# Kernel optimization log

Hardware: AMD Instinct MI355X
Metric: run time of the kernel (lower is better)

The kernel has to match this reference:

```python
import jax, jax.numpy as jnp
import numpy as np

H = 4   # num_attention_heads
C = 32  # attention_head_size
LN_EPS = 1e-5

def setup_inputs() -> dict:
    key = jax.random.key(0)
    ks = jax.random.split(key, 8)
    E = 128  # embedding_channels; all_head_size = H*C = 128
    B, I, J = 1, 256, 256
    s = 1.0 / np.sqrt(E)
    return {
        "z": jax.random.normal(ks[0], (B, I, J, E), dtype=jnp.float32),
        "ln_scale": jnp.ones((E,), jnp.float32),
        "ln_bias": jnp.zeros((E,), jnp.float32),
        # weights stored as [in, out] (torch Linear applies x @ W.T; here y = x @ W)
        "Wq": jax.random.normal(ks[1], (E, H * C), jnp.float32) * s,
        "Wk": jax.random.normal(ks[2], (E, H * C), jnp.float32) * s,
        "Wv": jax.random.normal(ks[3], (E, H * C), jnp.float32) * s,
        "Wg": jax.random.normal(ks[4], (E, H * C), jnp.float32) * s,
        "bg": jnp.zeros((H * C,), jnp.float32),
        "Wo": jax.random.normal(ks[5], (H * C, E), jnp.float32) * s,
        "bo": jnp.zeros((E,), jnp.float32),
    }

def reference(z, ln_scale, ln_bias, Wq, Wk, Wv, Wg, bg, Wo, bo):
    B, I, J, E = z.shape
    # LayerNorm over last dim
    mu = jnp.mean(z, axis=-1, keepdims=True)
    var = jnp.mean(jnp.square(z - mu), axis=-1, keepdims=True)
    zn = (z - mu) * jax.lax.rsqrt(var + LN_EPS) * ln_scale + ln_bias
    # QKV projections, reshaped to heads: [B, I, J, H, C]
    q = (zn @ Wq).reshape(B, I, J, H, C)
    k = (zn @ Wk).reshape(B, I, J, H, C)
    v = (zn @ Wv).reshape(B, I, J, H, C)
    # Row-wise attention (NOTE: original has no 1/sqrt(c) scaling)
    logits = jnp.einsum('biqhc,bikhc->bihqk', q, k)  # [B, I, H, J, J]
    weights = jax.nn.softmax(logits, axis=-1)
    wavg = jnp.einsum('bihqk,bikhc->biqhc', weights, v)  # [B, I, J, H, C]
    # Sigmoid gate
    g = jax.nn.sigmoid((zn @ Wg + bg).reshape(B, I, J, H, C))
    out = (g * wavg).reshape(B, I, J, H * C)
    return out @ Wo + bo
```

## Files before the change

kernel.cpp:

```cpp
#include <hip/hip_runtime.h>

typedef unsigned short u16;
typedef unsigned int   u32;
using bf16x8 = __attribute__((ext_vector_type(8))) __bf16;
using f32x4  = __attribute__((ext_vector_type(4))) float;

#define MFMA16(a,b,c) __builtin_amdgcn_mfma_f32_16x16x32_bf16(a,b,c,0,0,0)

__device__ __forceinline__ float b2f(u16 u){ u32 x = ((u32)u) << 16; return __builtin_bit_cast(float, x); }
__device__ __forceinline__ u16 f2b(float f){
    u32 x = __builtin_bit_cast(u32, f);
    return (u16)((x + 0x7fffu + ((x >> 16) & 1u)) >> 16);
}
__device__ __forceinline__ u32 pk2(float a, float b){ return (u32)f2b(a) | ((u32)f2b(b) << 16); }

constexpr int LDB = 136;
constexpr int LDK = 40;
constexpr int LDV = 264;
constexpr int LDQ = 40;
constexpr int LDZ = 136;
constexpr int LDT = 20;

__global__ __launch_bounds__(256) void kw_prep(
    const float* __restrict__ Wq, const float* __restrict__ Wk,
    const float* __restrict__ Wv, const float* __restrict__ Wg,
    const float* __restrict__ Wo, u16* __restrict__ Wt)
{
    const int m = blockIdx.x >> 4;
    const int r = ((blockIdx.x & 15) << 8) | threadIdx.x;
    const int o  = r >> 5;
    const int e4 = (r & 31) << 2;
    const float* __restrict__ src;
    bool lo = false;
    switch (m) {
        case 0: src = Wq; break;
        case 1: src = Wk; break;
        case 2: src = Wv; break;
        case 3: src = Wg; break;
        case 4: src = Wq; lo = true; break;
        case 5: src = Wk; lo = true; break;
        default: src = Wo; break;
    }
    float w[4];
    #pragma unroll
    for (int i = 0; i < 4; ++i) w[i] = src[(e4 + i) * 128 + o];
    if (lo) {
        #pragma unroll
        for (int i = 0; i < 4; ++i) w[i] -= b2f(f2b(w[i]));
    }
    uint2 outv;
    outv.x = pk2(w[0], w[1]);
    outv.y = pk2(w[2], w[3]);
    *(uint2*)(Wt + m * 16384 + o * 128 + e4) = outv;
}

__global__ __launch_bounds__(512, 2) void k1_proj(
    const float* __restrict__ z, const float* __restrict__ lns, const float* __restrict__ lnb,
    const u16* __restrict__ Wt, const float* __restrict__ bg,
    u16* __restrict__ Qo, u16* __restrict__ Ko, u16* __restrict__ Vo, u16* __restrict__ Go)
{
    __shared__ __attribute__((aligned(16))) u16 bufA[128 * LDB];
    __shared__ __attribute__((aligned(16))) u16 bufB[128 * LDB];
    __shared__ __attribute__((aligned(16))) u16 ett[8 * 16 * LDT];

    const int t = threadIdx.x;
    const int lane = t & 63;
    const int l15  = lane & 15;
    const int quad = lane >> 4;
    const int wave = t >> 6;
    const int rowbase = blockIdx.x * 128 + wave * 16;
    u16* __restrict__ lntile = bufA + wave * 16 * LDZ;
    u16* __restrict__ myE = ett + wave * 16 * LDT;

    bf16x8 zfh[4], zfl[4];
    {
        float sc[32], bi[32];
        #pragma unroll
        for (int u = 0; u < 8; ++u) {
            float4 s4 = *(const float4*)(lns + quad * 32 + u * 4);
            float4 b4 = *(const float4*)(lnb + quad * 32 + u * 4);
            sc[u*4+0]=s4.x; sc[u*4+1]=s4.y; sc[u*4+2]=s4.z; sc[u*4+3]=s4.w;
            bi[u*4+0]=b4.x; bi[u*4+1]=b4.y; bi[u*4+2]=b4.z; bi[u*4+3]=b4.w;
        }
        const size_t tok = (size_t)(rowbase + l15);
        float x[32];
        #pragma unroll
        for (int u = 0; u < 8; ++u) {
            float4 v4 = *(const float4*)(z + (tok << 7) + quad * 32 + u * 4);
            x[u*4+0]=v4.x; x[u*4+1]=v4.y; x[u*4+2]=v4.z; x[u*4+3]=v4.w;
        }
        float s = 0.f;
        #pragma unroll
        for (int k = 0; k < 32; ++k) s += x[k];
        s += __shfl_xor(s, 16, 64); s += __shfl_xor(s, 32, 64);
        const float mu = s * 0.0078125f;
        float vs = 0.f;
        #pragma unroll
        for (int k = 0; k < 32; ++k) { float d = x[k] - mu; vs += d * d; }
        vs += __shfl_xor(vs, 16, 64); vs += __shfl_xor(vs, 32, 64);
        const float rs = rsqrtf(vs * 0.0078125f + 1e-5f);
        float y[32];
        #pragma unroll
        for (int k = 0; k < 32; ++k) y[k] = (x[k] - mu) * rs * sc[k] + bi[k];
        #pragma unroll
        for (int u = 0; u < 4; ++u) {
            uint4 o;
            o.x = pk2(y[u*8+0], y[u*8+1]); o.y = pk2(y[u*8+2], y[u*8+3]);
            o.z = pk2(y[u*8+4], y[u*8+5]); o.w = pk2(y[u*8+6], y[u*8+7]);
            *(uint4*)(lntile + l15 * LDZ + quad * 32 + u * 8) = o;
        }
        #pragma unroll
        for (int ks = 0; ks < 4; ++ks)
            zfh[ks] = *(const bf16x8*)(lntile + l15 * LDZ + ks * 32 + quad * 8);
        #pragma unroll
        for (int k = 0; k < 32; ++k) y[k] -= b2f(f2b(y[k]));
        #pragma unroll
        for (int u = 0; u < 4; ++u) {
            uint4 o;
            o.x = pk2(y[u*8+0], y[u*8+1]); o.y = pk2(y[u*8+2], y[u*8+3]);
            o.z = pk2(y[u*8+4], y[u*8+5]); o.w = pk2(y[u*8+6], y[u*8+7]);
            *(uint4*)(lntile + l15 * LDZ + quad * 32 + u * 8) = o;
        }
        #pragma unroll
        for (int ks = 0; ks < 4; ++ks)
            zfl[ks] = *(const bf16x8*)(lntile + l15 * LDZ + ks * 32 + quad * 8);
    }

    auto stage = [&](u16* __restrict__ buf, const u16* __restrict__ src) {
        #pragma unroll
        for (int u = 0; u < 4; ++u) {
            const int c = (t + u * 512) * 8;
            *(uint4*)(buf + (c >> 7) * LDB + (c & 127)) = *(const uint4*)(src + c);
        }
    };

    u16* Os[4] = {Qo, Ko, Vo, Go};

    #pragma unroll 1
    for (int g = 0; g < 4; ++g) {
        __syncthreads();
        stage(bufA, Wt + g * 16384);
        const bool three = (g < 2);
        if (three) stage(bufB, Wt + (4 + g) * 16384);
        __syncthreads();
        u16* __restrict__ O = Os[g];
        #pragma unroll
        for (int nt = 0; nt < 8; ++nt) {
            f32x4 ac = {0.f, 0.f, 0.f, 0.f};
            const int bbase = (nt * 16 + l15) * LDB + quad * 8;
            #pragma unroll
            for (int ks = 0; ks < 4; ++ks) {
                bf16x8 bh = *(const bf16x8*)(bufA + bbase + ks * 32);
                ac = MFMA16(zfh[ks], bh, ac);
                if (three) {
                    bf16x8 bl = *(const bf16x8*)(bufB + bbase + ks * 32);
                    ac = MFMA16(zfl[ks], bh, ac);
                    ac = MFMA16(zfh[ks], bl, ac);
                }
            }
            const int col = nt * 16 + l15;
            #pragma unroll
            for (int r = 0; r < 4; ++r) {
                float v = ac[r];
                if (g == 3) v = 1.f / (1.f + __expf(-(v + bg[col])));
                myE[(quad * 4 + r) * LDT + l15] = f2b(v);
            }
            uint2 w = *(const uint2*)(myE + l15 * LDT + quad * 4);
            *(uint2*)(O + ((size_t)(rowbase + l15) << 7) + nt * 16 + quad * 4) = w;
        }
    }
}

__global__ __launch_bounds__(512, 4) void k2_attn(
    u16* QG, const u16* __restrict__ K, const u16* __restrict__ V)
{
    __shared__ __attribute__((aligned(16))) u16 kh[256 * 64];
    __shared__ __attribute__((aligned(16))) u16 vt[64 * LDV];
    __shared__ __attribute__((aligned(16))) u16 ptt[8 * 16 * LDQ];

    const int bid = blockIdx.x;
    const int i = bid >> 1, hp = bid & 1;
    const int t = threadIdx.x;
    const int lane = t & 63;
    const int l15  = lane & 15;
    const int quad = lane >> 4;
    const int wave = t >> 6;
    u16* __restrict__ myT = ptt + wave * 16 * LDQ;
    const size_t rb = ((size_t)i) << 8;
    const int cb = hp * 64;

    {
        const int tok = t >> 1, half = t & 1;
        const int swz = (tok & 7) << 3;
        const u16* ksrc = K + ((rb + tok) << 7) + cb + half * 32;
        #pragma unroll
        for (int u = 0; u < 4; ++u)
            *(uint4*)(kh + tok * 64 + ((half * 32 + u * 8) ^ swz)) = *(const uint4*)(ksrc + u * 8);
        const u16* vsrc = V + ((rb + tok) << 7) + cb + half * 32;
        #pragma unroll
        for (int u = 0; u < 4; ++u) {
            uint4 q = *(const uint4*)(vsrc + u * 8);
            u32 w4[4] = {q.x, q.y, q.z, q.w};
            #pragma unroll
            for (int k2 = 0; k2 < 4; ++k2) {
                vt[(half * 32 + u * 8 + k2 * 2    ) * LDV + tok] = (u16)(w4[k2] & 0xffffu);
                vt[(half * 32 + u * 8 + k2 * 2 + 1) * LDV + tok] = (u16)(w4[k2] >> 16);
            }
        }
    }
    __syncthreads();

    #pragma unroll 1
    for (int it = 0; it < 2; ++it) {
        u32 gwlo[2][4], gwhi[2][4];
        #pragma unroll
        for (int hh = 0; hh < 2; ++hh) {
            const int hc = cb + hh * 32;
            bf16x8 aq = *(const bf16x8*)(QG + ((rb + wave * 32 + it * 16 + l15) << 7) + hc + quad * 8);

            f32x4 s[16];
            #pragma unroll
            for (int nt = 0; nt < 16; ++nt) {
                const int key = nt * 16 + l15;
                bf16x8 b = *(const bf16x8*)(kh + key * 64 + ((hh * 32 + quad * 8) ^ ((key & 7) << 3)));
                f32x4 zacc = {0.f, 0.f, 0.f, 0.f};
                s[nt] = MFMA16(aq, b, zacc);
            }
            float inv[4];
            #pragma unroll
            for (int r = 0; r < 4; ++r) {
                float mx = s[0][r];
                #pragma unroll
                for (int nt = 1; nt < 16; ++nt) mx = fmaxf(mx, s[nt][r]);
                #pragma unroll
                for (int m = 1; m < 16; m <<= 1) mx = fmaxf(mx, __shfl_xor(mx, m, 64));
                float sm = 0.f;
                #pragma unroll
                for (int nt = 0; nt < 16; ++nt) {
                    float e = __expf(s[nt][r] - mx);
                    s[nt][r] = e; sm += e;
                }
                #pragma unroll
                for (int m = 1; m < 16; m <<= 1) sm += __shfl_xor(sm, m, 64);
                inv[r] = 1.f / sm;
            }
            f32x4 o0 = {0.f,0.f,0.f,0.f}, o1 = {0.f,0.f,0.f,0.f};
            #pragma unroll
            for (int c8 = 0; c8 < 8; ++c8) {
                #pragma unroll
                for (int n2 = 0; n2 < 2; ++n2)
                    #pragma unroll
                    for (int r = 0; r < 4; ++r)
                        myT[(quad * 4 + r) * LDQ + n2 * 16 + l15] = f2b(s[c8 * 2 + n2][r]);
                bf16x8 a  = *(const bf16x8*)(myT + l15 * LDQ + quad * 8);
                bf16x8 b0 = *(const bf16x8*)(vt + (hh * 32 +      l15) * LDV + c8 * 32 + quad * 8);
                bf16x8 b1 = *(const bf16x8*)(vt + (hh * 32 + 16 + l15) * LDV + c8 * 32 + quad * 8);
                o0 = MFMA16(a, b0, o0);
                o1 = MFMA16(a, b1, o1);
            }
            #pragma unroll
            for (int r = 0; r < 4; ++r) {
                gwlo[hh][r] = f2b(o0[r] * inv[r]);
                gwhi[hh][r] = f2b(o1[r] * inv[r]);
            }
        }
        #pragma unroll
        for (int r = 0; r < 4; ++r) {
            u16* dst = QG + ((rb + wave * 32 + it * 16 + quad * 4 + r) << 7) + cb;
            dst[     l15] = (u16)gwlo[0][r];
            dst[16 + l15] = (u16)gwhi[0][r];
            dst[32 + l15] = (u16)gwlo[1][r];
            dst[48 + l15] = (u16)gwhi[1][r];
        }
    }
}

__global__ __launch_bounds__(256, 4) void k3_out(
    const u16* __restrict__ GW, const u16* __restrict__ Gb,
    const u16* __restrict__ WoT, const float* __restrict__ bo,
    float* __restrict__ out)
{
    __shared__ __attribute__((aligned(16))) u16 wt[128 * LDB];
    __shared__ __attribute__((aligned(16))) float ftt[4 * 16 * LDT];
    const int t = threadIdx.x;
    const int lane = t & 63;
    const int l15  = lane & 15;
    const int quad = lane >> 4;
    const int wave = t >> 6;
    const int rowbase = blockIdx.x * 64 + wave * 16;
    float* __restrict__ myF = ftt + wave * 16 * LDT;

    #pragma unroll
    for (int u = 0; u < 8; ++u) {
        const int c = (t + u * 256) * 8;
        *(uint4*)(wt + (c >> 7) * LDB + (c & 127)) = *(const uint4*)(WoT + c);
    }
    bf16x8 af[4];
    {
        const size_t rowoff = (size_t)(rowbase + l15) << 7;
        #pragma unroll
        for (int ks = 0; ks < 4; ++ks) {
            bf16x8 a = *(const bf16x8*)(GW + rowoff + ks * 32 + quad * 8);
            bf16x8 g = *(const bf16x8*)(Gb + rowoff + ks * 32 + quad * 8);
            const u32* au = (const u32*)&a;
            const u32* gu = (const u32*)&g;
            u32 w[4];
            #pragma unroll
            for (int j = 0; j < 4; ++j) {
                float lo = b2f((u16)(au[j] & 0xffffu)) * b2f((u16)(gu[j] & 0xffffu));
                float hi = b2f((u16)(au[j] >> 16))     * b2f((u16)(gu[j] >> 16));
                w[j] = pk2(lo, hi);
            }
            af[ks] = *(const bf16x8*)w;
        }
    }
    __syncthreads();

    #pragma unroll
    for (int nt = 0; nt < 8; ++nt) {
        f32x4 ac = {0.f, 0.f, 0.f, 0.f};
        const int bbase = (nt * 16 + l15) * LDB + quad * 8;
        #pragma unroll
        for (int ks = 0; ks < 4; ++ks) {
            bf16x8 b = *(const bf16x8*)(wt + bbase + ks * 32);
            ac = MFMA16(af[ks], b, ac);
        }
        const float bb = bo[nt * 16 + l15];
        #pragma unroll
        for (int r = 0; r < 4; ++r)
            myF[(quad * 4 + r) * LDT + l15] = ac[r] + bb;
        float4 w = *(const float4*)(myF + l15 * LDT + quad * 4);
        *(float4*)(out + ((size_t)(rowbase + l15) << 7) + nt * 16 + quad * 4) = w;
    }
}

constexpr int FLDZ = 136;
constexpr int FLDW = 136;
constexpr int FLDO = 40;

__global__ __launch_bounds__(512, 2) void k_fused(
    const float* __restrict__ z, const float* __restrict__ lns, const float* __restrict__ lnb,
    const float* __restrict__ Wq, const float* __restrict__ Wk, const float* __restrict__ Wv,
    const float* __restrict__ Wg, const float* __restrict__ bg,
    const float* __restrict__ Wo, const float* __restrict__ bo,
    float* __restrict__ out)
{
    __shared__ __attribute__((aligned(16))) u16 smem[33280];
    const int i = blockIdx.x;
    const int t = threadIdx.x;
    const int lane = t & 63;
    const int l15  = lane & 15;
    const int quad = lane >> 4;
    const int wave = t >> 6;
    u16* __restrict__ kh   = smem;
    u16* __restrict__ vt   = smem + 10240;
    u16* __restrict__ bufA = smem + 18688;
    u16* __restrict__ myT  = smem + 23808 + wave * 16 * LDQ;
    u16* __restrict__ bufB = smem + 28928;
    u16* __restrict__ lntile = smem + wave * 16 * FLDZ;

    float4 wregA[2], wregB[2];
    auto prefW = [&](const float* __restrict__ W, int h, float4 (&r)[2]) {
        #pragma unroll
        for (int k2 = 0; k2 < 2; ++k2) {
            const int c = t * 4 + k2 * 2048;
            r[k2] = *(const float4*)(W + (c >> 5) * 128 + h * 32 + (c & 31));
        }
    };
    auto prefWoF = [&](int h, float4 (&r)[2]) {
        #pragma unroll
        for (int k2 = 0; k2 < 2; ++k2)
            r[k2] = *(const float4*)(Wo + h * 4096 + t * 4 + k2 * 2048);
    };
    auto stageHi = [&](u16* __restrict__ buf, const float4 (&r)[2]) {
        #pragma unroll
        for (int k2 = 0; k2 < 2; ++k2) {
            const int c = t * 4 + k2 * 2048;
            const int e = c >> 5, o = c & 31;
            buf[(o    ) * FLDW + e] = f2b(r[k2].x);
            buf[(o + 1) * FLDW + e] = f2b(r[k2].y);
            buf[(o + 2) * FLDW + e] = f2b(r[k2].z);
            buf[(o + 3) * FLDW + e] = f2b(r[k2].w);
        }
    };
    auto stageLo = [&](u16* __restrict__ buf, const float4 (&r)[2]) {
        #pragma unroll
        for (int k2 = 0; k2 < 2; ++k2) {
            const int c = t * 4 + k2 * 2048;
            const int e = c >> 5, o = c & 31;
            const float v0 = r[k2].x, v1 = r[k2].y, v2 = r[k2].z, v3 = r[k2].w;
            buf[(o    ) * FLDW + e] = f2b(v0 - b2f(f2b(v0)));
            buf[(o + 1) * FLDW + e] = f2b(v1 - b2f(f2b(v1)));
            buf[(o + 2) * FLDW + e] = f2b(v2 - b2f(f2b(v2)));
            buf[(o + 3) * FLDW + e] = f2b(v3 - b2f(f2b(v3)));
        }
    };
    auto stageWoL = [&](const float4 (&r)[2]) {
        #pragma unroll
        for (int k2 = 0; k2 < 2; ++k2) {
            const int c = t * 4 + k2 * 2048;
            const int kk = c >> 7, n = c & 127;
            bufA[(n    ) * FLDO + kk] = f2b(r[k2].x);
            bufA[(n + 1) * FLDO + kk] = f2b(r[k2].y);
            bufA[(n + 2) * FLDO + kk] = f2b(r[k2].z);
            bufA[(n + 3) * FLDO + kk] = f2b(r[k2].w);
        }
    };
    prefW(Wq, 0, wregA);
    bf16x8 zfh[2][4], zfl[2][4];
    {
        float sc[32], bi[32];
        #pragma unroll
        for (int u = 0; u < 8; ++u) {
            float4 s4 = *(const float4*)(lns + quad * 32 + u * 4);
            float4 b4 = *(const float4*)(lnb + quad * 32 + u * 4);
            sc[u*4+0]=s4.x; sc[u*4+1]=s4.y; sc[u*4+2]=s4.z; sc[u*4+3]=s4.w;
            bi[u*4+0]=b4.x; bi[u*4+1]=b4.y; bi[u*4+2]=b4.z; bi[u*4+3]=b4.w;
        }
        #pragma unroll 1
        for (int ms = 0; ms < 2; ++ms) {
            const size_t tok = (size_t)(i * 256 + wave * 32 + ms * 16 + l15);
            float x[32];
            #pragma unroll
            for (int u = 0; u < 8; ++u) {
                float4 v4 = *(const float4*)(z + (tok << 7) + quad * 32 + u * 4);
                x[u*4+0]=v4.x; x[u*4+1]=v4.y; x[u*4+2]=v4.z; x[u*4+3]=v4.w;
            }
            float s = 0.f;
            #pragma unroll
            for (int k = 0; k < 32; ++k) s += x[k];
            s += __shfl_xor(s, 16, 64); s += __shfl_xor(s, 32, 64);
            const float mu = s * 0.0078125f;
            float vs = 0.f;
            #pragma unroll
            for (int k = 0; k < 32; ++k) { float d = x[k] - mu; vs += d * d; }
            vs += __shfl_xor(vs, 16, 64); vs += __shfl_xor(vs, 32, 64);
            const float rs = rsqrtf(vs * 0.0078125f + 1e-5f);
            float y[32];
            #pragma unroll
            for (int k = 0; k < 32; ++k) y[k] = (x[k] - mu) * rs * sc[k] + bi[k];
            #pragma unroll
            for (int u = 0; u < 4; ++u) {
                uint4 o;
                o.x = pk2(y[u*8+0], y[u*8+1]); o.y = pk2(y[u*8+2], y[u*8+3]);
                o.z = pk2(y[u*8+4], y[u*8+5]); o.w = pk2(y[u*8+6], y[u*8+7]);
                *(uint4*)(lntile + l15 * FLDZ + quad * 32 + u * 8) = o;
            }
            #pragma unroll
            for (int ks = 0; ks < 4; ++ks)
                zfh[ms][ks] = *(const bf16x8*)(lntile + l15 * FLDZ + ks * 32 + quad * 8);
            #pragma unroll
            for (int k = 0; k < 32; ++k) y[k] -= b2f(f2b(y[k]));
            #pragma unroll
            for (int u = 0; u < 4; ++u) {
                uint4 o;
                o.x = pk2(y[u*8+0], y[u*8+1]); o.y = pk2(y[u*8+2], y[u*8+3]);
                o.z = pk2(y[u*8+4], y[u*8+5]); o.w = pk2(y[u*8+6], y[u*8+7]);
                *(uint4*)(lntile + l15 * FLDZ + quad * 32 + u * 8) = o;
            }
            #pragma unroll
            for (int ks = 0; ks < 4; ++ks)
                zfl[ms][ks] = *(const bf16x8*)(lntile + l15 * FLDZ + ks * 32 + quad * 8);
        }
    }
    __syncthreads();
    auto gemmAcc = [&](f32x4 (&acc)[2][2], bf16x8 (&af)[2][4], const u16* __restrict__ buf) {
        #pragma unroll
        for (int ms = 0; ms < 2; ++ms)
            #pragma unroll
            for (int nt = 0; nt < 2; ++nt) {
                f32x4 ac = acc[ms][nt];
                #pragma unroll
                for (int ks = 0; ks < 4; ++ks) {
                    bf16x8 b = *(const bf16x8*)(buf + (nt * 16 + l15) * FLDW + ks * 32 + quad * 8);
                    ac = MFMA16(af[ms][ks], b, ac);
                }
                acc[ms][nt] = ac;
            }
    };
    auto zero22 = [](f32x4 (&a)[2][2]) {
        #pragma unroll
        for (int ms = 0; ms < 2; ++ms)
            #pragma unroll
            for (int nt = 0; nt < 2; ++nt) a[ms][nt] = f32x4{0.f,0.f,0.f,0.f};
    };
    bf16x8 aq[2];
    f32x4  ga[2][2];
    f32x4  oacc[2][8];
    #pragma unroll
    for (int ms = 0; ms < 2; ++ms)
        #pragma unroll
        for (int nt = 0; nt < 8; ++nt)
            oacc[ms][nt] = f32x4{0.f, 0.f, 0.f, 0.f};
    #pragma unroll 1
    for (int h = 0; h < 4; ++h) {
        stageHi(bufA, wregA); stageLo(bufB, wregA);
        __syncthreads();
        prefW(Wk, h, wregA);
        {
            f32x4 qa[2][2]; zero22(qa);
            gemmAcc(qa, zfh, bufA); gemmAcc(qa, zfl, bufA); gemmAcc(qa, zfh, bufB);
            #pragma unroll
            for (int ms = 0; ms < 2; ++ms) {
                #pragma unroll
                for (int nt = 0; nt < 2; ++nt)
                    #pragma unroll
                    for (int r = 0; r < 4; ++r)
                        myT[(quad * 4 + r) * LDQ + nt * 16 + l15] = f2b(qa[ms][nt][r]);
                aq[ms] = *(const bf16x8*)(myT + l15 * LDQ + quad * 8);
            }
        }
        __syncthreads();
        stageHi(bufA, wregA); stageLo(bufB, wregA);
        __syncthreads();
        prefW(Wv, h, wregA); prefW(Wg, h, wregB);
        {
            f32x4 ka[2][2]; zero22(ka);
            gemmAcc(ka, zfh, bufA); gemmAcc(ka, zfl, bufA); gemmAcc(ka, zfh, bufB);
            #pragma unroll
            for (int ms = 0; ms < 2; ++ms)
                #pragma unroll
                for (int nt = 0; nt < 2; ++nt)
                    #pragma unroll
                    for (int r = 0; r < 4; ++r)
                        kh[(wave * 32 + ms * 16 + quad * 4 + r) * LDK + nt * 16 + l15] = f2b(ka[ms][nt][r]);
        }
        __syncthreads();
        stageHi(bufA, wregA); stageHi(bufB, wregB);
        __syncthreads();
        prefWoF(h, wregA);
        {
            f32x4 va[2][2]; zero22(va); gemmAcc(va, zfh, bufA);
            #pragma unroll
            for (int ms = 0; ms < 2; ++ms)
                #pragma unroll
                for (int nt = 0; nt < 2; ++nt)
                    #pragma unroll
                    for (int r = 0; r < 4; ++r)
                        vt[(nt * 16 + l15) * LDV + wave * 32 + ms * 16 + quad * 4 + r] = f2b(va[ms][nt][r]);
            zero22(ga); gemmAcc(ga, zfh, bufB);
            #pragma unroll
            for (int nt = 0; nt < 2; ++nt) {
                const float bb = bg[h * 32 + nt * 16 + l15];
                #pragma unroll
                for (int ms = 0; ms < 2; ++ms)
                    #pragma unroll
                    for (int r = 0; r < 4; ++r)
                        ga[ms][nt][r] = 1.f / (1.f + __expf(-(ga[ms][nt][r] + bb)));
            }
        }
        __syncthreads();
        stageWoL(wregA);
        __syncthreads();
        if (h < 3) prefW(Wq, h + 1, wregA);
        #pragma unroll 1
        for (int it = 0; it < 2; ++it) {
            f32x4 s[16];
            #pragma unroll
            for (int nt = 0; nt < 16; ++nt) {
                bf16x8 b = *(const bf16x8*)(kh + (nt * 16 + l15) * LDK + quad * 8);
                f32x4 zacc = {0.f, 0.f, 0.f, 0.f};
                s[nt] = MFMA16(aq[it], b, zacc);
            }
            float inv[4];
            #pragma unroll
            for (int r = 0; r < 4; ++r) {
                float mx = s[0][r];
                #pragma unroll
                for (int nt = 1; nt < 16; ++nt) mx = fmaxf(mx, s[nt][r]);
                #pragma unroll
                for (int m = 1; m < 16; m <<= 1) mx = fmaxf(mx, __shfl_xor(mx, m, 64));
                float sm = 0.f;
                #pragma unroll
                for (int nt = 0; nt < 16; ++nt) {
                    float e = __expf(s[nt][r] - mx);
                    s[nt][r] = e; sm += e;
                }
                #pragma unroll
                for (int m = 1; m < 16; m <<= 1) sm += __shfl_xor(sm, m, 64);
                inv[r] = 1.f / sm;
            }
            f32x4 o0 = {0.f,0.f,0.f,0.f}, o1 = {0.f,0.f,0.f,0.f};
            #pragma unroll
            for (int c8 = 0; c8 < 8; ++c8) {
                #pragma unroll
                for (int n2 = 0; n2 < 2; ++n2)
                    #pragma unroll
                    for (int r = 0; r < 4; ++r)
                        myT[(quad * 4 + r) * LDQ + n2 * 16 + l15] = f2b(s[c8 * 2 + n2][r]);
                bf16x8 a  = *(const bf16x8*)(myT + l15 * LDQ + quad * 8);
                bf16x8 b0 = *(const bf16x8*)(vt + (     l15) * LDV + c8 * 32 + quad * 8);
                bf16x8 b1 = *(const bf16x8*)(vt + (16 + l15) * LDV + c8 * 32 + quad * 8);
                o0 = MFMA16(a, b0, o0);
                o1 = MFMA16(a, b1, o1);
            }
            #pragma unroll
            for (int r = 0; r < 4; ++r) {
                myT[(quad * 4 + r) * LDQ + l15]      = f2b(o0[r] * inv[r] * ga[it][0][r]);
                myT[(quad * 4 + r) * LDQ + 16 + l15] = f2b(o1[r] * inv[r] * ga[it][1][r]);
            }
            bf16x8 agw = *(const bf16x8*)(myT + l15 * LDQ + quad * 8);
            #pragma unroll
            for (int nt = 0; nt < 8; ++nt) {
                bf16x8 bwo = *(const bf16x8*)(bufA + (nt * 16 + l15) * FLDO + quad * 8);
                oacc[it][nt] = MFMA16(agw, bwo, oacc[it][nt]);
            }
        }
        __syncthreads();
    }
    #pragma unroll
    for (int ms = 0; ms < 2; ++ms) {
        #pragma unroll
        for (int nt = 0; nt < 8; ++nt) {
            const int col = nt * 16 + l15;
            const float bb = bo[col];
            #pragma unroll
            for (int r = 0; r < 4; ++r) {
                const size_t row = (size_t)(i * 256 + wave * 32 + ms * 16 + quad * 4 + r);
                out[(row << 7) + col] = oacc[ms][nt][r] + bb;
            }
        }
    }
}

extern "C" void kernel_launch(void* const* d_in, const int* in_sizes, int n_in,
                              void* d_out, int out_size, void* d_ws, size_t ws_size,
                              hipStream_t stream)
{
    const float* z   = (const float*)d_in[0];
    const float* lns = (const float*)d_in[1];
    const float* lnb = (const float*)d_in[2];
    const float* Wq  = (const float*)d_in[3];
    const float* Wk  = (const float*)d_in[4];
    const float* Wv  = (const float*)d_in[5];
    const float* Wg  = (const float*)d_in[6];
    const float* bg  = (const float*)d_in[7];
    const float* Wo  = (const float*)d_in[8];
    const float* bo  = (const float*)d_in[9];
    float* out = (float*)d_out;

    const size_t NEED = 4ull * 65536 * 128 * 2 + 7ull * 16384 * 2;
    if (ws_size >= NEED) {
        u16* Qb = (u16*)d_ws;
        u16* Kb = Qb + 65536ull * 128;
        u16* Vb = Kb + 65536ull * 128;
        u16* Gb = Vb + 65536ull * 128;
        u16* Wt = Gb + 65536ull * 128;
        kw_prep<<<112, 256, 0, stream>>>(Wq, Wk, Wv, Wg, Wo, Wt);
        k1_proj<<<512, 512, 0, stream>>>(z, lns, lnb, Wt, bg, Qb, Kb, Vb, Gb);
        k2_attn<<<512, 512, 0, stream>>>(Qb, Kb, Vb);
        k3_out<<<1024, 256, 0, stream>>>(Qb, Gb, Wt + 6 * 16384, bo, out);
    } else {
        k_fused<<<256, 512, 0, stream>>>(z, lns, lnb, Wq, Wk, Wv, Wg, bg, Wo, bo, out);
    }
}
```

Baseline: 172.4 us.

## Process two row tiles per wave in projection kernel to reuse weight fragments

```diff
diff --git a/kernel.cpp b/kernel.cpp
--- a/kernel.cpp
+++ b/kernel.cpp
@@ -54,25 +54,23 @@
     *(uint2*)(Wt + m * 16384 + o * 128 + e4) = outv;
 }
 
-__global__ __launch_bounds__(512, 2) void k1_proj(
+__global__ __launch_bounds__(256, 2) void k1_proj(
     const float* __restrict__ z, const float* __restrict__ lns, const float* __restrict__ lnb,
     const u16* __restrict__ Wt, const float* __restrict__ bg,
     u16* __restrict__ Qo, u16* __restrict__ Ko, u16* __restrict__ Vo, u16* __restrict__ Go)
 {
     __shared__ __attribute__((aligned(16))) u16 bufA[128 * LDB];
     __shared__ __attribute__((aligned(16))) u16 bufB[128 * LDB];
-    __shared__ __attribute__((aligned(16))) u16 ett[8 * 16 * LDT];
 
     const int t = threadIdx.x;
     const int lane = t & 63;
     const int l15  = lane & 15;
     const int quad = lane >> 4;
     const int wave = t >> 6;
-    const int rowbase = blockIdx.x * 128 + wave * 16;
+    const int rowbase = blockIdx.x * 128 + wave * 32;
     u16* __restrict__ lntile = bufA + wave * 16 * LDZ;
-    u16* __restrict__ myE = ett + wave * 16 * LDT;
-
-    bf16x8 zfh[4], zfl[4];
+
+    bf16x8 zfh[2][4], zfl[2][4];
     {
         float sc[32], bi[32];
         #pragma unroll
@@ -82,54 +80,57 @@
             sc[u*4+0]=s4.x; sc[u*4+1]=s4.y; sc[u*4+2]=s4.z; sc[u*4+3]=s4.w;
             bi[u*4+0]=b4.x; bi[u*4+1]=b4.y; bi[u*4+2]=b4.z; bi[u*4+3]=b4.w;
         }
-        const size_t tok = (size_t)(rowbase + l15);
-        float x[32];
+        #pragma unroll 1
+        for (int ms = 0; ms < 2; ++ms) {
+            const size_t tok = (size_t)(rowbase + ms * 16 + l15);
+            float x[32];
+            #pragma unroll
+            for (int u = 0; u < 8; ++u) {
+                float4 v4 = *(const float4*)(z + (tok << 7) + quad * 32 + u * 4);
+                x[u*4+0]=v4.x; x[u*4+1]=v4.y; x[u*4+2]=v4.z; x[u*4+3]=v4.w;
+            }
+            float s = 0.f;
+            #pragma unroll
+            for (int k = 0; k < 32; ++k) s += x[k];
+            s += __shfl_xor(s, 16, 64); s += __shfl_xor(s, 32, 64);
+            const float mu = s * 0.0078125f;
+            float vs = 0.f;
+            #pragma unroll
+            for (int k = 0; k < 32; ++k) { float d = x[k] - mu; vs += d * d; }
+            vs += __shfl_xor(vs, 16, 64); vs += __shfl_xor(vs, 32, 64);
+            const float rs = rsqrtf(vs * 0.0078125f + 1e-5f);
+            float y[32];
+            #pragma unroll
+            for (int k = 0; k < 32; ++k) y[k] = (x[k] - mu) * rs * sc[k] + bi[k];
+            #pragma unroll
+            for (int u = 0; u < 4; ++u) {
+                uint4 o;
+                o.x = pk2(y[u*8+0], y[u*8+1]); o.y = pk2(y[u*8+2], y[u*8+3]);
+                o.z = pk2(y[u*8+4], y[u*8+5]); o.w = pk2(y[u*8+6], y[u*8+7]);
+                *(uint4*)(lntile + l15 * LDZ + quad * 32 + u * 8) = o;
+            }
+            #pragma unroll
+            for (int ks = 0; ks < 4; ++ks)
+                zfh[ms][ks] = *(const bf16x8*)(lntile + l15 * LDZ + ks * 32 + quad * 8);
+            #pragma unroll
+            for (int k = 0; k < 32; ++k) y[k] -= b2f(f2b(y[k]));
+            #pragma unroll
+            for (int u = 0; u < 4; ++u) {
+                uint4 o;
+                o.x = pk2(y[u*8+0], y[u*8+1]); o.y = pk2(y[u*8+2], y[u*8+3]);
+                o.z = pk2(y[u*8+4], y[u*8+5]); o.w = pk2(y[u*8+6], y[u*8+7]);
+                *(uint4*)(lntile + l15 * LDZ + quad * 32 + u * 8) = o;
+            }
+            #pragma unroll
+            for (int ks = 0; ks < 4; ++ks)
+                zfl[ms][ks] = *(const bf16x8*)(lntile + l15 * LDZ + ks * 32 + quad * 8);
+        }
+    }
+
+    auto stage = [&](u16* __restrict__ buf, const u16* __restrict__ src) {
         #pragma unroll
         for (int u = 0; u < 8; ++u) {
-            float4 v4 = *(const float4*)(z + (tok << 7) + quad * 32 + u * 4);
-            x[u*4+0]=v4.x; x[u*4+1]=v4.y; x[u*4+2]=v4.z; x[u*4+3]=v4.w;
-        }
-        float s = 0.f;
-        #pragma unroll
-        for (int k = 0; k < 32; ++k) s += x[k];
-        s += __shfl_xor(s, 16, 64); s += __shfl_xor(s, 32, 64);
-        const float mu = s * 0.0078125f;
-        float vs = 0.f;
-        #pragma unroll
-        for (int k = 0; k < 32; ++k) { float d = x[k] - mu; vs += d * d; }
-        vs += __shfl_xor(vs, 16, 64); vs += __shfl_xor(vs, 32, 64);
-        const float rs = rsqrtf(vs * 0.0078125f + 1e-5f);
-        float y[32];
-        #pragma unroll
-        for (int k = 0; k < 32; ++k) y[k] = (x[k] - mu) * rs * sc[k] + bi[k];
-        #pragma unroll
-        for (int u = 0; u < 4; ++u) {
-            uint4 o;
-            o.x = pk2(y[u*8+0], y[u*8+1]); o.y = pk2(y[u*8+2], y[u*8+3]);
-            o.z = pk2(y[u*8+4], y[u*8+5]); o.w = pk2(y[u*8+6], y[u*8+7]);
-            *(uint4*)(lntile + l15 * LDZ + quad * 32 + u * 8) = o;
-        }
-        #pragma unroll
-        for (int ks = 0; ks < 4; ++ks)
-            zfh[ks] = *(const bf16x8*)(lntile + l15 * LDZ + ks * 32 + quad * 8);
-        #pragma unroll
-        for (int k = 0; k < 32; ++k) y[k] -= b2f(f2b(y[k]));
-        #pragma unroll
-        for (int u = 0; u < 4; ++u) {
-            uint4 o;
-            o.x = pk2(y[u*8+0], y[u*8+1]); o.y = pk2(y[u*8+2], y[u*8+3]);
-            o.z = pk2(y[u*8+4], y[u*8+5]); o.w = pk2(y[u*8+6], y[u*8+7]);
-            *(uint4*)(lntile + l15 * LDZ + quad * 32 + u * 8) = o;
-        }
-        #pragma unroll
-        for (int ks = 0; ks < 4; ++ks)
-            zfl[ks] = *(const bf16x8*)(lntile + l15 * LDZ + ks * 32 + quad * 8);
-    }
-
-    auto stage = [&](u16* __restrict__ buf, const u16* __restrict__ src) {
-        #pragma unroll
-        for (int u = 0; u < 4; ++u) {
-            const int c = (t + u * 512) * 8;
+            const int c = (t + u * 256) * 8;
             *(uint4*)(buf + (c >> 7) * LDB + (c & 127)) = *(const uint4*)(src + c);
         }
     };
@@ -146,27 +147,34 @@
         u16* __restrict__ O = Os[g];
         #pragma unroll
         for (int nt = 0; nt < 8; ++nt) {
-            f32x4 ac = {0.f, 0.f, 0.f, 0.f};
+            f32x4 ac0 = {0.f, 0.f, 0.f, 0.f};
+            f32x4 ac1 = {0.f, 0.f, 0.f, 0.f};
             const int bbase = (nt * 16 + l15) * LDB + quad * 8;
             #pragma unroll
             for (int ks = 0; ks < 4; ++ks) {
                 bf16x8 bh = *(const bf16x8*)(bufA + bbase + ks * 32);
-                ac = MFMA16(zfh[ks], bh, ac);
+                ac0 = MFMA16(zfh[0][ks], bh, ac0);
+                ac1 = MFMA16(zfh[1][ks], bh, ac1);
                 if (three) {
                     bf16x8 bl = *(const bf16x8*)(bufB + bbase + ks * 32);
-                    ac = MFMA16(zfl[ks], bh, ac);
-                    ac = MFMA16(zfh[ks], bl, ac);
+                    ac0 = MFMA16(zfl[0][ks], bh, ac0);
+                    ac0 = MFMA16(zfh[0][ks], bl, ac0);
+                    ac1 = MFMA16(zfl[1][ks], bh, ac1);
+                    ac1 = MFMA16(zfh[1][ks], bl, ac1);
                 }
             }
             const int col = nt * 16 + l15;
+            const float gb = (g == 3) ? bg[col] : 0.f;
             #pragma unroll
             for (int r = 0; r < 4; ++r) {
-                float v = ac[r];
-                if (g == 3) v = 1.f / (1.f + __expf(-(v + bg[col])));
-                myE[(quad * 4 + r) * LDT + l15] = f2b(v);
-            }
-            uint2 w = *(const uint2*)(myE + l15 * LDT + quad * 4);
-            *(uint2*)(O + ((size_t)(rowbase + l15) << 7) + nt * 16 + quad * 4) = w;
+                float v0 = ac0[r], v1 = ac1[r];
+                if (g == 3) {
+                    v0 = 1.f / (1.f + __expf(-(v0 + gb)));
+                    v1 = 1.f / (1.f + __expf(-(v1 + gb)));
+                }
+                O[((size_t)(rowbase +      quad * 4 + r) << 7) + col] = f2b(v0);
+                O[((size_t)(rowbase + 16 + quad * 4 + r) << 7) + col] = f2b(v1);
+            }
         }
     }
 }
@@ -647,7 +655,7 @@
         u16* Gb = Vb + 65536ull * 128;
         u16* Wt = Gb + 65536ull * 128;
         kw_prep<<<112, 256, 0, stream>>>(Wq, Wk, Wv, Wg, Wo, Wt);
-        k1_proj<<<512, 512, 0, stream>>>(z, lns, lnb, Wt, bg, Qb, Kb, Vb, Gb);
+        k1_proj<<<512, 256, 0, stream>>>(z, lns, lnb, Wt, bg, Qb, Kb, Vb, Gb);
         k2_attn<<<512, 512, 0, stream>>>(Qb, Kb, Vb);
         k3_out<<<1024, 256, 0, stream>>>(Qb, Gb, Wt + 6 * 16384, bo, out);
     } else {
```

After: 219.7 us. 27.4% more time.
